# Kernel optimization log

Measured on AMD Instinct MI355X. Metric: run time of the kernel, lower is better.

## Reference

```python
import jax, jax.numpy as jnp
import numpy as np

N, E, C, F = 20000, 320000, 64, 8
DIN = 2 * C + F + 1           # MLP input: sender scalars + receiver scalars + radial feats + length
AVG = 16.0                    # avg_num_neighbors
INV_SQRT3 = 0.5773502691896258


def setup_inputs() -> dict:
    key = jax.random.key(0)
    ks = jax.random.split(key, 16)
    d = {}
    d["node_feats"] = jax.random.normal(ks[0], (N, C + 3 * C), jnp.float32)  # 64x0e + 64x1o (mul-major)
    d["edge_attrs"] = jax.random.normal(ks[1], (E, 4), jnp.float32)           # SH: 1x0e + 1x1o
    d["edge_feats"] = jax.random.normal(ks[2], (E, F), jnp.float32)           # radial basis
    d["lengths"] = jax.random.uniform(ks[3], (E, 1), jnp.float32)
    d["edge_index"] = jax.random.randint(ks[4], (2, E), 0, N, jnp.int32)      # (sender, receiver)
    d["Wsc"] = jax.random.normal(ks[5], (C, C), jnp.float32) / np.sqrt(C).astype(np.float32)
    d["Wup0"] = jax.random.normal(ks[6], (C, C), jnp.float32) / np.sqrt(C).astype(np.float32)
    d["Wup1"] = jax.random.normal(ks[7], (C, C), jnp.float32) / np.sqrt(C).astype(np.float32)
    d["W1"] = jax.random.normal(ks[8], (DIN, C), jnp.float32) / np.sqrt(DIN).astype(np.float32)
    d["b1"] = jnp.zeros((C,), jnp.float32)
    d["W2"] = jax.random.normal(ks[9], (C, C), jnp.float32) / np.sqrt(C).astype(np.float32)
    d["b2"] = jnp.zeros((C,), jnp.float32)
    d["W3"] = jax.random.normal(ks[10], (C, 4 * C), jnp.float32) * 1e-3       # near-zero init like the source
    d["Ws"] = jax.random.normal(ks[11], (2 * C, C), jnp.float32) / np.sqrt(2 * C).astype(np.float32)
    d["Wv"] = jax.random.normal(ks[12], (2 * C, C), jnp.float32) / np.sqrt(2 * C).astype(np.float32)
    return d


def reference(node_feats, edge_attrs, edge_feats, lengths, edge_index,
              Wsc, Wup0, Wup1, W1, b1, W2, b2, W3, Ws, Wv):
    n = node_feats.shape[0]
    s = node_feats[:, :C]                          # [N,C] scalar (0e) channels
    v = node_feats[:, C:].reshape(n, C, 3)         # [N,C,3] vector (1o) channels

    node_scalars = s @ Wsc                          # linear_scalar -> 64x0e
    s_up = s @ Wup0                                 # linear_up, 0e block
    v_up = jnp.einsum('nci,cd->ndi', v, Wup1)       # linear_up, 1o block

    snd, rcv = edge_index[0], edge_index[1]

    # weight MLP: Dense->silu->Dense->silu->Dense(no bias)
    mlp_in = jnp.concatenate([node_scalars[snd], node_scalars[rcv], edge_feats, lengths], axis=-1)
    h = jax.nn.silu(mlp_in @ W1 + b1)
    h = jax.nn.silu(h @ W2 + b2)
    tw = h @ W3                                     # [E, 4C] per-irrep tp weights
    w0, w1, w2, w3 = jnp.split(tw, 4, axis=-1)

    y0 = edge_attrs[:, :1]                          # [E,1] SH l=0
    y1 = edge_attrs[:, 1:4]                         # [E,3] SH l=1
    xs = s_up[snd]                                  # [E,C]   gather senders
    xv = v_up[snd]                                  # [E,C,3]

    # weighted tensor product paths (component normalization), filtered to 0e/1o
    p0 = xs * y0 * w0                                               # 0e x 0e -> 0e  [E,C]
    p1 = (jnp.einsum('eci,ei->ec', xv, y1) * INV_SQRT3) * w1        # 1o x 1o -> 0e  [E,C]
    p2 = xs[:, :, None] * y1[:, None, :] * w2[:, :, None]           # 0e x 1o -> 1o  [E,C,3]
    p3 = xv * y0[:, :, None] * w3[:, :, None]                       # 1o x 0e -> 1o  [E,C,3]

    # scatter_sum messages into receiver nodes
    m0 = jax.ops.segment_sum(jnp.concatenate([p0, p1], axis=-1), rcv, num_segments=n)  # [N,2C]
    m1 = jax.ops.segment_sum(jnp.concatenate([p2, p3], axis=1), rcv, num_segments=n)   # [N,2C,3]

    # final equivariant linear on simplified irreps_mid (128x0e + 128x1o), / avg_num_neighbors
    out_s = (m0 @ Ws) / AVG                          # [N,C]
    out_v = jnp.einsum('nci,cd->ndi', m1, Wv) / AVG  # [N,C,3]

    # reshape_irreps -> [N, channels, 1 + 3]
    return jnp.concatenate([out_s[:, :, None], out_v], axis=-1)
```

## Files before the change

kernel.cpp:

```cpp
#include <hip/hip_runtime.h>

#define N_NODES 20000
#define N_EDGES 320000
#define INV_SQRT3 0.5773502691896258f

typedef unsigned short u16;
typedef unsigned int u32;
typedef __attribute__((ext_vector_type(8))) short short8;
typedef __attribute__((ext_vector_type(4))) float f32x4;
typedef __attribute__((ext_vector_type(4))) u32 u32x4v;

static const size_t OFF_NSBF = 0;
static const size_t OFF_SV   = 2560000;
static const size_t OFF_MG   = 23040000;
static const size_t OFF_TW   = 64000000;
static const size_t OFF_W1F  = 227840000;
static const size_t OFF_W2F  = 227860480;
static const size_t OFF_W3F  = 227868672;
static const size_t OFF_WNF  = 227901440;
static const size_t OFF_CNT  = 227950592;
static const size_t OFF_OFFS = 228030592;
static const size_t OFF_CUR  = 228110608;
static const size_t OFF_ES   = 228190608;
static const size_t OFF_SS   = 229470608;
static const size_t OFF_RS   = 230750608;

static __device__ __forceinline__ u16 f2bf(float x) {
    union { float f; u32 u; } c; c.f = x;
    u32 u = c.u + 0x7fffu + ((c.u >> 16) & 1u);
    return (u16)(u >> 16);
}
static __device__ __forceinline__ float bf2f(u16 b) {
    union { u32 u; float f; } c; c.u = (u32)b << 16; return c.f;
}
static __device__ __forceinline__ u16 f2h(float x) {
    union { _Float16 h; u16 u; } c; c.h = (_Float16)x; return c.u;
}
static __device__ __forceinline__ float h2f(u32 b) {
    union { u16 u; _Float16 h; } c; c.u = (u16)b; return (float)c.h;
}
static __device__ __forceinline__ f32x4 mfma16(short8 a, short8 b, f32x4 c) {
    return __builtin_amdgcn_mfma_f32_16x16x32_bf16(a, b, c, 0, 0, 0);
}
static __device__ __forceinline__ float silu(float x) {
    return x / (1.0f + __expf(-x));
}
template <typename T>
static __device__ __forceinline__ T ntload(const T* p) { return __builtin_nontemporal_load(p); }
template <typename T>
static __device__ __forceinline__ void ntstore(T* p, T v) { __builtin_nontemporal_store(v, p); }

__global__ void prep_w_kernel(const float* __restrict__ W1, const float* __restrict__ W2,
                              const float* __restrict__ W3,
                              u16* __restrict__ W1f, u16* __restrict__ W2f, u16* __restrict__ W3f) {
    int t = blockIdx.x * 256 + threadIdx.x;
    if (t >= 3840) return;
    int l = t & 63, grp = t >> 6;
    int hi = l >> 4, lo = l & 15;
    if (grp < 20) {
        int kk = grp >> 2, jt = grp & 3;
#pragma unroll
        for (int e2 = 0; e2 < 8; e2++) {
            int k = kk * 32 + hi * 8 + e2, j = jt * 16 + lo;
            W1f[(size_t)(grp * 64 + l) * 8 + e2] = (k < 137) ? f2bf(W1[k * 64 + j]) : (u16)0;
        }
    } else if (grp < 28) {
        int g = grp - 20; int kk = g >> 2, jt = g & 3;
#pragma unroll
        for (int e2 = 0; e2 < 8; e2++) {
            int k = kk * 32 + hi * 8 + e2, j = jt * 16 + lo;
            W2f[(size_t)(g * 64 + l) * 8 + e2] = f2bf(W2[k * 64 + j]);
        }
    } else {
        int g = grp - 28; int kk = g >> 4, jt = g & 15;
#pragma unroll
        for (int e2 = 0; e2 < 8; e2++) {
            int k = kk * 32 + hi * 8 + e2, j = jt * 16 + lo;
            W3f[(size_t)(g * 64 + l) * 8 + e2] = f2bf(W3[k * 256 + j]);
        }
    }
}

__global__ void prep_wn_kernel(const float* __restrict__ Wsc, const float* __restrict__ Wup0,
                               const float* __restrict__ Wup1, u16* __restrict__ WNF) {
    int t = blockIdx.x * 256 + threadIdx.x;
    if (t >= 1536) return;
    int mat = t >> 9;
    int rem = t & 511;
    int g = rem >> 6, l = rem & 63;
    int kk = g >> 2, jt = g & 3, hi = l >> 4, lo = l & 15;
    const float* W = (mat == 0) ? Wsc : (mat == 1) ? Wup0 : Wup1;
    u16* dh = WNF + (size_t)mat * 8192 + (size_t)(g * 64 + l) * 8;
    u16* dl = dh + 4096;
#pragma unroll
    for (int e2 = 0; e2 < 8; e2++) {
        int k = kk * 32 + hi * 8 + e2, d = jt * 16 + lo;
        float w = W[k * 64 + d];
        u16 h = f2bf(w);
        dh[e2] = h;
        dl[e2] = f2bf(w - bf2f(h));
    }
}

__global__ void prep_w2_kernel(const float* __restrict__ Ws, const float* __restrict__ Wv,
                               u16* __restrict__ WSF) {
    int t = blockIdx.x * 256 + threadIdx.x;
    if (t >= 2048) return;
    int l = t & 63, grp = t >> 6;
    int wsel = grp >> 4;
    int g = grp & 15;
    int kk = g >> 2, jt = g & 3;
    int hi = l >> 4, lo = l & 15;
    const float* W = wsel ? Wv : Ws;
    u16* dh = WSF + (size_t)wsel * 16384;
    u16* dl = dh + 8192;
    size_t base = (size_t)(g * 64 + l) * 8;
#pragma unroll
    for (int e2 = 0; e2 < 8; e2++) {
        int k = kk * 32 + hi * 8 + e2, d = jt * 16 + lo;
        float w = W[k * 64 + d];
        u16 h = f2bf(w);
        float r = w - bf2f(h);
        dh[base + e2] = h;
        dl[base + e2] = f2bf(r);
    }
}

__global__ __launch_bounds__(256) void node_prep_kernel(
    const float* __restrict__ node_feats, const u16* __restrict__ WNF,
    u16* __restrict__ ns_bf, f32x4* __restrict__ sv) {
    const int tid = threadIdx.x;
    const int lane = tid & 63;
    const int w = tid >> 6;
    const int lo16 = lane & 15;
    const int hi = lane >> 4;
    const int nb = blockIdx.x * 64 + w * 16;

    int an = nb + lo16; if (an > N_NODES - 1) an = N_NODES - 1;
    const float* arow = node_feats + (size_t)an * 256;

    const short8* B = (const short8*)WNF;

    f32x4 acc_ns[4], acc_su[4], acc_v[3][4];
#pragma unroll
    for (int jt = 0; jt < 4; jt++) {
        acc_ns[jt] = (f32x4)(0.0f);
        acc_su[jt] = (f32x4)(0.0f);
#pragma unroll
        for (int i = 0; i < 3; i++) acc_v[i][jt] = (f32x4)(0.0f);
    }

#pragma unroll
    for (int kk = 0; kk < 2; kk++) {
        short8 sh, sl;
        {
            const float* sp = arow + kk * 32 + hi * 8;
            f32x4 x0 = *(const f32x4*)sp;
            f32x4 x1 = *(const f32x4*)(sp + 4);
#pragma unroll
            for (int j = 0; j < 4; j++) {
                u16 h0 = f2bf(x0[j]);
                sh[j] = (short)h0;
                sl[j] = (short)f2bf(x0[j] - bf2f(h0));
                u16 h1 = f2bf(x1[j]);
                sh[4 + j] = (short)h1;
                sl[4 + j] = (short)f2bf(x1[j] - bf2f(h1));
            }
        }
        short8 vh[3], vl[3];
#pragma unroll
        for (int i = 0; i < 3; i++) {
            const float* vp = arow + 64 + i + 3 * (kk * 32 + hi * 8);
#pragma unroll
            for (int e = 0; e < 8; e++) {
                float x = vp[e * 3];
                u16 hb = f2bf(x);
                vh[i][e] = (short)hb;
                vl[i][e] = (short)f2bf(x - bf2f(hb));
            }
        }
#pragma unroll
        for (int jt = 0; jt < 4; jt++) {
            int fi = (kk * 4 + jt) * 64 + lane;
            short8 bh = B[fi], bl = B[512 + fi];
            acc_ns[jt] = mfma16(sh, bh, acc_ns[jt]);
            acc_ns[jt] = mfma16(sl, bh, acc_ns[jt]);
            acc_ns[jt] = mfma16(sh, bl, acc_ns[jt]);
            bh = B[1024 + fi]; bl = B[1536 + fi];
            acc_su[jt] = mfma16(sh, bh, acc_su[jt]);
            acc_su[jt] = mfma16(sl, bh, acc_su[jt]);
            acc_su[jt] = mfma16(sh, bl, acc_su[jt]);
            bh = B[2048 + fi]; bl = B[2560 + fi];
#pragma unroll
            for (int i = 0; i < 3; i++) {
                acc_v[i][jt] = mfma16(vh[i], bh, acc_v[i][jt]);
                acc_v[i][jt] = mfma16(vl[i], bh, acc_v[i][jt]);
                acc_v[i][jt] = mfma16(vh[i], bl, acc_v[i][jt]);
            }
        }
    }

#pragma unroll
    for (int r = 0; r < 4; r++) {
        int n = nb + hi * 4 + r;
        if (n < N_NODES) {
#pragma unroll
            for (int jt = 0; jt < 4; jt++) {
                int d = jt * 16 + lo16;
                ns_bf[(size_t)n * 64 + d] = f2bf(acc_ns[jt][r]);
                f32x4 o;
                o.x = acc_su[jt][r];
                o.y = acc_v[0][jt][r];
                o.z = acc_v[1][jt][r];
                o.w = acc_v[2][jt][r];
                sv[(size_t)n * 64 + d] = o;
            }
        }
    }
}

__global__ void hist_kernel(const int* __restrict__ ei, int* __restrict__ cnt) {
    int e = blockIdx.x * 256 + threadIdx.x;
    if (e < N_EDGES) atomicAdd(&cnt[ei[N_EDGES + e]], 1);
}

__global__ void scan_kernel(const int* __restrict__ cnt, int* __restrict__ offs,
                            int* __restrict__ cursor) {
    __shared__ int buf[1024];
    int t = threadIdx.x;
    int base = t * 20;
    int loc[20];
    int tot = 0;
#pragma unroll
    for (int i = 0; i < 20; i++) {
        int idx = base + i;
        int v = (idx < N_NODES) ? cnt[idx] : 0;
        loc[i] = tot;
        tot += v;
    }
    buf[t] = tot;
    __syncthreads();
    for (int d = 1; d < 1024; d <<= 1) {
        int add = (t >= d) ? buf[t - d] : 0;
        __syncthreads();
        buf[t] += add;
        __syncthreads();
    }
    int ebase = buf[t] - tot;
#pragma unroll
    for (int i = 0; i < 20; i++) {
        int idx = base + i;
        if (idx < N_NODES) { int o = ebase + loc[i]; offs[idx] = o; cursor[idx] = o; }
    }
    if (t == 1023) offs[N_NODES] = buf[1023];
}

__global__ void scatter_kernel(const int* __restrict__ ei, int* __restrict__ cursor,
                               int* __restrict__ esort, int* __restrict__ ssort,
                               int* __restrict__ rsort) {
    int e = blockIdx.x * 256 + threadIdx.x;
    if (e < N_EDGES) {
        int sn = ei[e];
        int rc = ei[N_EDGES + e];
        int pos = atomicAdd(&cursor[rc], 1);
        esort[pos] = e;
        ssort[pos] = sn;
        rsort[pos] = rc;
    }
}

__global__ __launch_bounds__(256, 4) void mlp_kernel(
    const u16* __restrict__ ns_bf,
    const u16* __restrict__ W1f, const u16* __restrict__ W2f, const u16* __restrict__ W3f,
    const float* __restrict__ b1, const float* __restrict__ b2,
    const float* __restrict__ edge_feats, const float* __restrict__ lengths,
    const int* __restrict__ esort, const int* __restrict__ ssort, const int* __restrict__ rsort,
    u16* __restrict__ twg) {

    __shared__ u16 mlp[64][168];
    __shared__ u16 h1s[64][72];
    __shared__ u16 h2s[64][72];

    const int tid = threadIdx.x;
    const int l = tid & 63;
    const int lo16 = l & 15;
    const int hi = l >> 4;
    const int w = tid >> 6;
    const int erow = (w << 4) | lo16;
    const int koff = hi * 8;
    const int drow = (w << 4) + hi * 4;

    const int p0 = blockIdx.x * 64;

    const short8* w1frag = (const short8*)W1f;
    const short8* w2frag = (const short8*)W2f;
    const short8* w3frag = (const short8*)W3f;

    float bb1[4], bb2[4];
#pragma unroll
    for (int jt = 0; jt < 4; jt++) { bb1[jt] = b1[jt * 16 + lo16]; bb2[jt] = b2[jt * 16 + lo16]; }

    {
        int rr = tid >> 2, pp = tid & 3;
        uint4 z = {0, 0, 0, 0};
        *(uint4*)&mlp[rr][136 + pp * 8] = z;
    }

    {
        int es = tid >> 2, part = tid & 3;
        int e = esort[p0 + es];
        int sn = ssort[p0 + es];
        int rc = rsort[p0 + es];
        const uint4* ps = (const uint4*)(ns_bf + (size_t)sn * 64 + part * 16);
        uint4 s0 = ps[0], s1 = ps[1];
        *(uint4*)&mlp[es][part * 16] = s0;
        *(uint4*)&mlp[es][part * 16 + 8] = s1;
        const uint4* pr = (const uint4*)(ns_bf + (size_t)rc * 64 + part * 16);
        uint4 r0v = pr[0], r1v = pr[1];
        *(uint4*)&mlp[es][64 + part * 16] = r0v;
        *(uint4*)&mlp[es][64 + part * 16 + 8] = r1v;
        if (part == 0) {
            float4 f0 = *(const float4*)(edge_feats + (size_t)e * 8);
            float4 f1 = *(const float4*)(edge_feats + (size_t)e * 8 + 4);
            u32 pk0 = (u32)f2bf(f0.x) | ((u32)f2bf(f0.y) << 16);
            u32 pk1 = (u32)f2bf(f0.z) | ((u32)f2bf(f0.w) << 16);
            u32 pk2 = (u32)f2bf(f1.x) | ((u32)f2bf(f1.y) << 16);
            u32 pk3 = (u32)f2bf(f1.z) | ((u32)f2bf(f1.w) << 16);
            uint4 pk = {pk0, pk1, pk2, pk3};
            *(uint4*)&mlp[es][128] = pk;
            mlp[es][136] = f2bf(lengths[e]);
        }
    }
    __syncthreads();

    f32x4 a1c[4];
#pragma unroll
    for (int jt = 0; jt < 4; jt++) a1c[jt] = (f32x4)(0.0f);
#pragma unroll
    for (int kk = 0; kk < 5; kk++) {
        short8 af = *(const short8*)&mlp[erow][kk * 32 + koff];
        const short8* wb = w1frag + kk * 256 + l;
        a1c[0] = mfma16(af, wb[0],   a1c[0]);
        a1c[1] = mfma16(af, wb[64],  a1c[1]);
        a1c[2] = mfma16(af, wb[128], a1c[2]);
        a1c[3] = mfma16(af, wb[192], a1c[3]);
    }
#pragma unroll
    for (int jt = 0; jt < 4; jt++) {
#pragma unroll
        for (int r = 0; r < 4; r++) {
            float x = a1c[jt][r] + bb1[jt];
            h1s[drow + r][jt * 16 + lo16] = f2bf(silu(x));
        }
    }
    __syncthreads();

    f32x4 a2c[4];
#pragma unroll
    for (int jt = 0; jt < 4; jt++) a2c[jt] = (f32x4)(0.0f);
#pragma unroll
    for (int kk = 0; kk < 2; kk++) {
        short8 af = *(const short8*)&h1s[erow][kk * 32 + koff];
        const short8* wb = w2frag + kk * 256 + l;
        a2c[0] = mfma16(af, wb[0],   a2c[0]);
        a2c[1] = mfma16(af, wb[64],  a2c[1]);
        a2c[2] = mfma16(af, wb[128], a2c[2]);
        a2c[3] = mfma16(af, wb[192], a2c[3]);
    }
#pragma unroll
    for (int jt = 0; jt < 4; jt++) {
#pragma unroll
        for (int r = 0; r < 4; r++) {
            float x = a2c[jt][r] + bb2[jt];
            h2s[drow + r][jt * 16 + lo16] = f2bf(silu(x));
        }
    }
    __syncthreads();

    f32x4 tw[16];
#pragma unroll
    for (int jt = 0; jt < 16; jt++) tw[jt] = (f32x4)(0.0f);
#pragma unroll
    for (int kk = 0; kk < 2; kk++) {
        short8 af = *(const short8*)&h2s[erow][kk * 32 + koff];
        const short8* wb = w3frag + kk * 1024 + l;
#pragma unroll
        for (int jt = 0; jt < 16; jt++) tw[jt] = mfma16(af, wb[jt * 64], tw[jt]);
    }

    int relrow = p0 + drow;
#pragma unroll
    for (int r = 0; r < 4; r++) {
        u32 q0a = (u32)f2h(tw[0][r])  | ((u32)f2h(tw[1][r])  << 16);
        u32 q0b = (u32)f2h(tw[2][r])  | ((u32)f2h(tw[3][r])  << 16);
        u32 q1a = (u32)f2h(tw[4][r])  | ((u32)f2h(tw[5][r])  << 16);
        u32 q1b = (u32)f2h(tw[6][r])  | ((u32)f2h(tw[7][r])  << 16);
        u32 q2a = (u32)f2h(tw[8][r])  | ((u32)f2h(tw[9][r])  << 16);
        u32 q2b = (u32)f2h(tw[10][r]) | ((u32)f2h(tw[11][r]) << 16);
        u32 q3a = (u32)f2h(tw[12][r]) | ((u32)f2h(tw[13][r]) << 16);
        u32 q3b = (u32)f2h(tw[14][r]) | ((u32)f2h(tw[15][r]) << 16);
        u16* dst = twg + (size_t)(relrow + r) * 256 + lo16 * 16;
        u32x4v A = {q0a, q0b, q1a, q1b};
        u32x4v B = {q2a, q2b, q3a, q3b};
        *(u32x4v*)dst = A;
        *(((u32x4v*)dst) + 1) = B;
    }
}

__global__ __launch_bounds__(256, 4) void seg_kernel(
    const f32x4* __restrict__ sv, const float* __restrict__ edge_attrs,
    const int* __restrict__ esort, const int* __restrict__ ssort,
    const int* __restrict__ offs, const u16* __restrict__ twg,
    float* __restrict__ m_g) {
    const int lane = threadIdx.x & 63;
    const int wv = threadIdx.x >> 6;
    const int n = blockIdx.x * 4 + wv;
    const int c = lane;
    const int jt = c >> 4, lo16 = c & 15;
    const int e0 = offs[n], e1 = offs[n + 1];
    float a_m0 = 0.f, a_m0b = 0.f;
    float a20 = 0.f, a21 = 0.f, a22 = 0.f, a30 = 0.f, a31 = 0.f, a32 = 0.f;
#pragma unroll 2
    for (int pos = e0; pos < e1; ++pos) {
        int e = esort[pos];
        int sn = ssort[pos];
        const u16* twp = twg + (size_t)pos * 256 + lo16 * 16;
        u32x4v ta = *((const u32x4v*)twp);
        u32x4v tb = *(((const u32x4v*)twp) + 1);
        f32x4 y4 = *(const f32x4*)(edge_attrs + (size_t)e * 4);
        f32x4 s4 = sv[(size_t)sn * 64 + c];
        u32 wwa = (jt & 2) ? ta.y : ta.x;
        u32 wwb = (jt & 2) ? ta.w : ta.z;
        u32 wwc = (jt & 2) ? tb.y : tb.x;
        u32 wwd = (jt & 2) ? tb.w : tb.z;
        int sh = (jt & 1) << 4;
        float w0 = h2f((wwa >> sh) & 0xffffu);
        float w1 = h2f((wwb >> sh) & 0xffffu);
        float w2 = h2f((wwc >> sh) & 0xffffu);
        float w3 = h2f((wwd >> sh) & 0xffffu);
        float xs = s4.x, xv0 = s4.y, xv1 = s4.z, xv2 = s4.w;
        float y0 = y4.x, ya = y4.y, yb = y4.z, yc = y4.w;
        a_m0 = fmaf(xs * y0, w0, a_m0);
        float dv = xv0 * ya + xv1 * yb + xv2 * yc;
        a_m0b = fmaf(dv, w1, a_m0b);
        float sw2 = xs * w2;
        a20 = fmaf(sw2, ya, a20); a21 = fmaf(sw2, yb, a21); a22 = fmaf(sw2, yc, a22);
        float yw3 = y0 * w3;
        a30 = fmaf(xv0, yw3, a30); a31 = fmaf(xv1, yw3, a31); a32 = fmaf(xv2, yw3, a32);
    }
    float* mr = m_g + (size_t)n * 512;
    ntstore(mr + c,        a_m0);
    ntstore(mr + 64 + c,   a_m0b * INV_SQRT3);
    ntstore(mr + 128 + c,  a20);
    ntstore(mr + 192 + c,  a30);
    ntstore(mr + 256 + c,  a21);
    ntstore(mr + 320 + c,  a31);
    ntstore(mr + 384 + c,  a22);
    ntstore(mr + 448 + c,  a32);
}

__global__ __launch_bounds__(256, 2) void out_kernel(
    const float* __restrict__ m_g, const u16* __restrict__ WSF,
    float* __restrict__ out) {
    const int tid = threadIdx.x;
    const int lane = tid & 63;
    const int w = tid >> 6;
    const int lo16 = lane & 15;
    const int hi = lane >> 4;
    const int nb = blockIdx.x * 64 + w * 16;

    int arow_n = nb + lo16;
    if (arow_n > N_NODES - 1) arow_n = N_NODES - 1;
    const float* arow = m_g + (size_t)arow_n * 512 + hi * 8;

    const short8* bsh = (const short8*)WSF;
    const short8* bsl = (const short8*)(WSF + 8192);
    const short8* bvh = (const short8*)(WSF + 16384);
    const short8* bvl = (const short8*)(WSF + 24576);

    f32x4 acc[4][4];
#pragma unroll
    for (int q = 0; q < 4; q++)
#pragma unroll
        for (int jt = 0; jt < 4; jt++) acc[q][jt] = (f32x4)(0.0f);

#pragma unroll
    for (int kk = 0; kk < 4; kk++) {
        short8 ahi[4], alo[4];
#pragma unroll
        for (int q = 0; q < 4; q++) {
            const float* p = arow + q * 128 + kk * 32;
            f32x4 x0 = ntload((const f32x4*)p);
            f32x4 x1 = ntload((const f32x4*)(p + 4));
#pragma unroll
            for (int j = 0; j < 4; j++) {
                u16 h0 = f2bf(x0[j]);
                ahi[q][j] = (short)h0;
                alo[q][j] = (short)f2bf(x0[j] - bf2f(h0));
                u16 h1 = f2bf(x1[j]);
                ahi[q][4 + j] = (short)h1;
                alo[q][4 + j] = (short)f2bf(x1[j] - bf2f(h1));
            }
        }
#pragma unroll
        for (int jt = 0; jt < 4; jt++) {
            int bidx = (kk * 4 + jt) * 64 + lane;
            short8 wh_s = bsh[bidx];
            short8 wl_s = bsl[bidx];
            short8 wh_v = bvh[bidx];
            short8 wl_v = bvl[bidx];
            acc[0][jt] = mfma16(ahi[0], wh_s, acc[0][jt]);
            acc[0][jt] = mfma16(alo[0], wh_s, acc[0][jt]);
            acc[0][jt] = mfma16(ahi[0], wl_s, acc[0][jt]);
#pragma unroll
            for (int q = 1; q < 4; q++) {
                acc[q][jt] = mfma16(ahi[q], wh_v, acc[q][jt]);
                acc[q][jt] = mfma16(alo[q], wh_v, acc[q][jt]);
                acc[q][jt] = mfma16(ahi[q], wl_v, acc[q][jt]);
            }
        }
    }

#pragma unroll
    for (int r = 0; r < 4; r++) {
        int n = nb + hi * 4 + r;
        if (n < N_NODES) {
#pragma unroll
            for (int jt = 0; jt < 4; jt++) {
                int d = jt * 16 + lo16;
                f32x4 o;
                o.x = acc[0][jt][r] * 0.0625f;
                o.y = acc[1][jt][r] * 0.0625f;
                o.z = acc[2][jt][r] * 0.0625f;
                o.w = acc[3][jt][r] * 0.0625f;
                ntstore((f32x4*)(out + (size_t)n * 256 + d * 4), o);
            }
        }
    }
}

extern "C" void kernel_launch(void* const* d_in, const int* in_sizes, int n_in,
                              void* d_out, int out_size, void* d_ws, size_t ws_size,
                              hipStream_t stream) {
    (void)in_sizes; (void)n_in; (void)out_size; (void)ws_size;
    const float* node_feats = (const float*)d_in[0];
    const float* edge_attrs = (const float*)d_in[1];
    const float* edge_feats = (const float*)d_in[2];
    const float* lengths    = (const float*)d_in[3];
    const int*   edge_index = (const int*)d_in[4];
    const float* Wsc  = (const float*)d_in[5];
    const float* Wup0 = (const float*)d_in[6];
    const float* Wup1 = (const float*)d_in[7];
    const float* W1   = (const float*)d_in[8];
    const float* b1   = (const float*)d_in[9];
    const float* W2   = (const float*)d_in[10];
    const float* b2   = (const float*)d_in[11];
    const float* W3   = (const float*)d_in[12];
    const float* Ws   = (const float*)d_in[13];
    const float* Wv   = (const float*)d_in[14];

    char* ws = (char*)d_ws;
    u16*   ns_bf  = (u16*)(ws + OFF_NSBF);
    f32x4* sv     = (f32x4*)(ws + OFF_SV);
    float* m_g    = (float*)(ws + OFF_MG);
    u16*   twg    = (u16*)(ws + OFF_TW);
    u16*   W1f    = (u16*)(ws + OFF_W1F);
    u16*   W2f    = (u16*)(ws + OFF_W2F);
    u16*   W3f    = (u16*)(ws + OFF_W3F);
    u16*   WNF    = (u16*)(ws + OFF_WNF);
    int*   cnt    = (int*)(ws + OFF_CNT);
    int*   offs   = (int*)(ws + OFF_OFFS);
    int*   cursor = (int*)(ws + OFF_CUR);
    u16*   WSF    = (u16*)(ws + OFF_CUR);
    int*   esort  = (int*)(ws + OFF_ES);
    int*   ssort  = (int*)(ws + OFF_SS);
    int*   rsort  = (int*)(ws + OFF_RS);
    float* out    = (float*)d_out;

    (void)hipMemsetAsync(cnt, 0, N_NODES * sizeof(int), stream);
    prep_w_kernel<<<15, 256, 0, stream>>>(W1, W2, W3, W1f, W2f, W3f);
    prep_wn_kernel<<<6, 256, 0, stream>>>(Wsc, Wup0, Wup1, WNF);
    node_prep_kernel<<<(N_NODES + 63) / 64, 256, 0, stream>>>(node_feats, WNF, ns_bf, sv);
    hist_kernel<<<N_EDGES / 256, 256, 0, stream>>>(edge_index, cnt);
    scan_kernel<<<1, 1024, 0, stream>>>(cnt, offs, cursor);
    scatter_kernel<<<N_EDGES / 256, 256, 0, stream>>>(edge_index, cursor, esort, ssort, rsort);
    prep_w2_kernel<<<8, 256, 0, stream>>>(Ws, Wv, WSF);

    mlp_kernel<<<N_EDGES / 64, 256, 0, stream>>>(ns_bf, W1f, W2f, W3f, b1, b2,
                                                 edge_feats, lengths,
                                                 esort, ssort, rsort, twg);
    seg_kernel<<<N_NODES / 4, 256, 0, stream>>>(sv, edge_attrs, esort, ssort,
                                                offs, twg, m_g);
    out_kernel<<<(N_NODES + 63) / 64, 256, 0, stream>>>(m_g, WSF, out);
}
```

Measured before the change: 266.5 us.

## Vectorize scan loads, alias MLP LDS buffers, raise occupancy, unroll segment loop

The scan kernel now reads its 20 counts per thread with int4 loads instead of scalar loads. The MLP kernel reuses the input staging buffer for the second hidden layer, which cuts LDS per block, and raises the launch-bounds min-blocks from 4 to 5 to allow more resident blocks. The segment-sum loop unroll goes from 2 to 4 to expose more memory-level parallelism. The higher occupancy target may force register spills in the MLP kernel, and the wider unroll raises register pressure in seg_kernel.

Measured after the change: 268.3 us. Within noise of the previous version (+0.7%).

```diff
diff --git a/kernel.cpp b/kernel.cpp
--- a/kernel.cpp
+++ b/kernel.cpp
@@ -231,13 +231,20 @@
     int base = t * 20;
     int loc[20];
     int tot = 0;
-#pragma unroll
-    for (int i = 0; i < 20; i++) {
-        int idx = base + i;
-        int v = (idx < N_NODES) ? cnt[idx] : 0;
-        loc[i] = tot;
-        tot += v;
-    }
+    int v20[20];
+    if (base < N_NODES) {
+#pragma unroll
+        for (int q = 0; q < 5; q++) {
+            int4 vv = *(const int4*)&cnt[base + q * 4];
+            v20[q * 4 + 0] = vv.x; v20[q * 4 + 1] = vv.y;
+            v20[q * 4 + 2] = vv.z; v20[q * 4 + 3] = vv.w;
+        }
+    } else {
+#pragma unroll
+        for (int i = 0; i < 20; i++) v20[i] = 0;
+    }
+#pragma unroll
+    for (int i = 0; i < 20; i++) { loc[i] = tot; tot += v20[i]; }
     buf[t] = tot;
     __syncthreads();
     for (int d = 1; d < 1024; d <<= 1) {
@@ -269,7 +276,7 @@
     }
 }
 
-__global__ __launch_bounds__(256, 4) void mlp_kernel(
+__global__ __launch_bounds__(256, 5) void mlp_kernel(
     const u16* __restrict__ ns_bf,
     const u16* __restrict__ W1f, const u16* __restrict__ W2f, const u16* __restrict__ W3f,
     const float* __restrict__ b1, const float* __restrict__ b2,
@@ -277,9 +284,9 @@
     const int* __restrict__ esort, const int* __restrict__ ssort, const int* __restrict__ rsort,
     u16* __restrict__ twg) {
 
-    __shared__ u16 mlp[64][168];
+    __shared__ u16 mlpbuf[64][168];
     __shared__ u16 h1s[64][72];
-    __shared__ u16 h2s[64][72];
+    u16* h2sf = &mlpbuf[0][0];
 
     const int tid = threadIdx.x;
     const int l = tid & 63;
@@ -303,7 +310,7 @@
     {
         int rr = tid >> 2, pp = tid & 3;
         uint4 z = {0, 0, 0, 0};
-        *(uint4*)&mlp[rr][136 + pp * 8] = z;
+        *(uint4*)&mlpbuf[rr][136 + pp * 8] = z;
     }
 
     {
@@ -313,12 +320,12 @@
         int rc = rsort[p0 + es];
         const uint4* ps = (const uint4*)(ns_bf + (size_t)sn * 64 + part * 16);
         uint4 s0 = ps[0], s1 = ps[1];
-        *(uint4*)&mlp[es][part * 16] = s0;
-        *(uint4*)&mlp[es][part * 16 + 8] = s1;
+        *(uint4*)&mlpbuf[es][part * 16] = s0;
+        *(uint4*)&mlpbuf[es][part * 16 + 8] = s1;
         const uint4* pr = (const uint4*)(ns_bf + (size_t)rc * 64 + part * 16);
         uint4 r0v = pr[0], r1v = pr[1];
-        *(uint4*)&mlp[es][64 + part * 16] = r0v;
-        *(uint4*)&mlp[es][64 + part * 16 + 8] = r1v;
+        *(uint4*)&mlpbuf[es][64 + part * 16] = r0v;
+        *(uint4*)&mlpbuf[es][64 + part * 16 + 8] = r1v;
         if (part == 0) {
             float4 f0 = *(const float4*)(edge_feats + (size_t)e * 8);
             float4 f1 = *(const float4*)(edge_feats + (size_t)e * 8 + 4);
@@ -327,8 +334,8 @@
             u32 pk2 = (u32)f2bf(f1.x) | ((u32)f2bf(f1.y) << 16);
             u32 pk3 = (u32)f2bf(f1.z) | ((u32)f2bf(f1.w) << 16);
             uint4 pk = {pk0, pk1, pk2, pk3};
-            *(uint4*)&mlp[es][128] = pk;
-            mlp[es][136] = f2bf(lengths[e]);
+            *(uint4*)&mlpbuf[es][128] = pk;
+            mlpbuf[es][136] = f2bf(lengths[e]);
         }
     }
     __syncthreads();
@@ -338,7 +345,7 @@
     for (int jt = 0; jt < 4; jt++) a1c[jt] = (f32x4)(0.0f);
 #pragma unroll
     for (int kk = 0; kk < 5; kk++) {
-        short8 af = *(const short8*)&mlp[erow][kk * 32 + koff];
+        short8 af = *(const short8*)&mlpbuf[erow][kk * 32 + koff];
         const short8* wb = w1frag + kk * 256 + l;
         a1c[0] = mfma16(af, wb[0],   a1c[0]);
         a1c[1] = mfma16(af, wb[64],  a1c[1]);
@@ -372,7 +379,7 @@
 #pragma unroll
         for (int r = 0; r < 4; r++) {
             float x = a2c[jt][r] + bb2[jt];
-            h2s[drow + r][jt * 16 + lo16] = f2bf(silu(x));
+            h2sf[(drow + r) * 72 + jt * 16 + lo16] = f2bf(silu(x));
         }
     }
     __syncthreads();
@@ -382,7 +389,7 @@
     for (int jt = 0; jt < 16; jt++) tw[jt] = (f32x4)(0.0f);
 #pragma unroll
     for (int kk = 0; kk < 2; kk++) {
-        short8 af = *(const short8*)&h2s[erow][kk * 32 + koff];
+        short8 af = *(const short8*)&h2sf[erow * 72 + kk * 32 + koff];
         const short8* wb = w3frag + kk * 1024 + l;
 #pragma unroll
         for (int jt = 0; jt < 16; jt++) tw[jt] = mfma16(af, wb[jt * 64], tw[jt]);
@@ -420,7 +427,7 @@
     const int e0 = offs[n], e1 = offs[n + 1];
     float a_m0 = 0.f, a_m0b = 0.f;
     float a20 = 0.f, a21 = 0.f, a22 = 0.f, a30 = 0.f, a31 = 0.f, a32 = 0.f;
-#pragma unroll 2
+#pragma unroll 4
     for (int pos = e0; pos < e1; ++pos) {
         int e = esort[pos];
         int sn = ssort[pos];
```
